# Optimization experiments

Measured on AMD Instinct MI355X. Metric: run time of the kernel, lower is better.

The kernel has to match this reference:

```python
import jax, jax.numpy as jnp
import numpy as np

SAMPLERATE = 22050
N_OCTAVES = 16
N_SAMPLES = 2 ** 15  # 32768
N_EVENTS = 64
BATCH = 4
MIN_HZ = 20
MAX_HZ = 3000
BASE_RESONANCE = 0.01

MIN_FREQ = MIN_HZ / (SAMPLERATE // 2)
MAX_FREQ = MAX_HZ / (SAMPLERATE // 2)
FREQ_RANGE = MAX_FREQ - MIN_FREQ


def setup_inputs() -> dict:
    key = jax.random.key(0)
    k1, k2, k3, k4 = jax.random.split(key, 4)
    return {
        "f0": jax.random.uniform(k1, (BATCH, N_EVENTS, 1), dtype=jnp.float32),
        "decay_coefficients": jax.random.normal(k2, (BATCH, N_EVENTS, 1), dtype=jnp.float32),
        "phase_offsets": jax.random.normal(k3, (BATCH, N_EVENTS, 1), dtype=jnp.float32),
        "freq_spacing": jax.random.uniform(k4, (BATCH, N_EVENTS, 1), dtype=jnp.float32),
    }


def reference(f0, decay_coefficients, phase_offsets, freq_spacing):
    b, e, _ = f0.shape
    f0 = jnp.abs(f0)  # (B, E, 1)

    # computed in the original forward but never used in the output
    _ = jax.nn.sigmoid(phase_offsets) * np.pi

    # exponential_decay(torch.sigmoid(decay_coefficients), ...) -> double sigmoid
    dv = jax.nn.sigmoid(jax.nn.sigmoid(decay_coefficients))  # (B, E, 1)
    resonance_factor = (1.0 - BASE_RESONANCE) * 0.95
    decay = BASE_RESONANCE + dv * resonance_factor
    log_decay = jnp.log(decay + 1e-12)
    # cumsum of the constant over n_frames = n_octaves; F.interpolate to the
    # same size (n_samples=n_octaves in the call) is an identity.
    exp_decays = jnp.exp(jnp.cumsum(
        jnp.broadcast_to(log_decay, (b, e, N_OCTAVES)), axis=-1))  # (B, E, O)

    f0 = (MIN_FREQ + f0 * FREQ_RANGE) * np.pi  # (B, E, 1)
    factors = jnp.cumsum(
        jnp.broadcast_to(freq_spacing, (b, e, N_OCTAVES)), axis=-1)  # (B, E, O)
    f0s = f0 * factors  # (B, E, O) per-octave angular increments

    # cumulative phase over samples, then sin oscillator bank
    phase = jnp.cumsum(
        jnp.broadcast_to(f0s[..., None], (b, e, N_OCTAVES, N_SAMPLES)), axis=-1)
    osc = jnp.sin(phase) * exp_decays[..., None]  # (B, E, O, S)
    osc = jnp.sum(osc, axis=2)  # (B, E, S)

    # max_norm along the sample dim
    mx = jnp.max(jnp.abs(osc), axis=-1, keepdims=True)
    return osc / (mx + 1e-8)
```

## Files before the change

### kernel.cpp

```cpp
#include <hip/hip_runtime.h>
#include <math.h>

#pragma clang fp contract(off)

constexpr int NSAMP = 32768;
constexpr int NROWS = 256;
constexpr int NOCT  = 16;
constexpr int TPB   = 1024;

__device__ __forceinline__ float keepf(float x) {
  asm volatile("" : "+v"(x));
  return x;
}

__global__ __launch_bounds__(TPB, 4) void f0res_kernel(
    const float* __restrict__ f0_in,
    const float* __restrict__ dec_in,
    const float* __restrict__ fs_in,
    float* __restrict__ out)
{
  const int row = blockIdx.x;
  const int t   = threadIdx.x;

  __shared__ float s_tab[NOCT][64];
  __shared__ float s_w[NOCT];
  __shared__ float s_osc[NSAMP];
  __shared__ float s_red[TPB / 64];

  const float f0a = fabsf(f0_in[row]);
  const float dcc = dec_in[row];
  const float fsv = fs_in[row];

  const float MIN_F = (float)(20.0 / 11025.0);
  const float RNG_F = (float)(3000.0 / 11025.0 - 20.0 / 11025.0);
  const float c1    = keepf(f0a * RNG_F);
  const float c2    = keepf(MIN_F + c1);
  const float f0ang = keepf(c2 * (float)M_PI);

  const float sg    = 1.0f / (1.0f + expf(-dcc));
  const float dvv   = 1.0f / (1.0f + expf(-sg));
  const float dvr   = keepf(dvv * 0.9405f);
  const float decay = keepf(0.01f + dvr);
  const float ldv   = logf(decay + 1e-12f);

  if (t < NOCT) {
    const int k = t;
    float fac = 0.0f;
    for (int j = 0; j <= k; ++j) fac = fac + fsv;
    const float x = keepf(f0ang * fac);
    float* tab = s_tab[k];
    float a = 0.0f;
#pragma unroll
    for (int i = 0; i < 16; ++i) { a = a + x;  tab[i]      = a; }
    const float T0 = a; a = 0.0f;
#pragma unroll
    for (int i = 0; i < 16; ++i) { a = a + T0; tab[16 + i] = a; }
    const float T1 = a; a = 0.0f;
#pragma unroll
    for (int i = 0; i < 16; ++i) { a = a + T1; tab[32 + i] = a; }
    const float T2 = a; a = 0.0f;
#pragma unroll
    for (int i = 0; i < 8;  ++i) { a = a + T2; tab[48 + i] = a; }
    float lc = 0.0f;
    for (int j = 0; j <= k; ++j) lc = lc + ldv;
    s_w[k] = expf(lc);
  }
  __syncthreads();

  const float C1 = 6.28125f;
  const float C2 = (float)(6.283185307179586476925287 - 6.28125);
  const float INV2PI = (float)0.159154943091895335768883;

  float lmax = 0.0f;

#pragma unroll
  for (int h = 0; h < 2; ++h) {
    const int m = 2 * t - 1 + h;
    float acc[16];
#pragma unroll
    for (int i = 0; i < 16; ++i) acc[i] = 0.0f;

    for (int k = 0; k < NOCT; ++k) {
      const float* tab = s_tab[k];
      float carry = 0.0f;
      if (m >= 0) {
        carry = tab[16 + (m & 15)];
        const int m2 = (m >> 4) - 1;
        if (m2 >= 0) {
          float p2 = tab[32 + (m2 & 15)];
          const int m3 = (m2 >> 4) - 1;
          if (m3 >= 0) p2 = p2 + tab[48 + m3];
          carry = carry + p2;
        }
      }
      const float w = s_w[k];
      float tv[16];
      *(float4*)&tv[0]  = ((const float4*)tab)[0];
      *(float4*)&tv[4]  = ((const float4*)tab)[1];
      *(float4*)&tv[8]  = ((const float4*)tab)[2];
      *(float4*)&tv[12] = ((const float4*)tab)[3];
#pragma unroll
      for (int i = 0; i < 16; ++i) {
        const float p = tv[i] + carry;
        const float kq = rintf(p * INV2PI);
        float r = __builtin_fmaf(-kq, C1, p);
        r = __builtin_fmaf(-kq, C2, r);
        const float fr = r * INV2PI;
        float sv;
        asm("v_sin_f32 %0, %1" : "=v"(sv) : "v"(fr));
        const float pr = w * sv;
        acc[i] = acc[i] + pr;
      }
    }
#pragma unroll
    for (int i = 0; i < 16; ++i) lmax = fmaxf(lmax, fabsf(acc[i]));
    float4* dst = (float4*)&s_osc[32 * t + 16 * h];
#pragma unroll
    for (int q = 0; q < 4; ++q) {
      float4 v;
      v.x = acc[4*q]; v.y = acc[4*q+1]; v.z = acc[4*q+2]; v.w = acc[4*q+3];
      dst[q] = v;
    }
  }

#pragma unroll
  for (int off = 32; off >= 1; off >>= 1)
    lmax = fmaxf(lmax, __shfl_xor(lmax, off, 64));
  if ((t & 63) == 0) s_red[t >> 6] = lmax;
  __syncthreads();
  float mx = s_red[0];
#pragma unroll
  for (int i = 1; i < TPB / 64; ++i) mx = fmaxf(mx, s_red[i]);
  const float inv = 1.0f / (mx + 1e-8f);

  float4* orow = (float4*)(out + (size_t)row * NSAMP);
  const float4* src = (const float4*)s_osc;
#pragma unroll
  for (int g = 0; g < 8; ++g) {
    float4 v = src[t + 1024 * g];
    v.x *= inv; v.y *= inv; v.z *= inv; v.w *= inv;
    orow[t + 1024 * g] = v;
  }
}

extern "C" void kernel_launch(void* const* d_in, const int* in_sizes, int n_in,
                              void* d_out, int out_size, void* d_ws, size_t ws_size,
                              hipStream_t stream) {
    const float* f0  = (const float*)d_in[0];
    const float* dcc = (const float*)d_in[1];
    const float* fsp = (const float*)d_in[3];
    float* out = (float*)d_out;

    f0res_kernel<<<NROWS, TPB, 0, stream>>>(f0, dcc, fsp, out);
}
```

Baseline: 48.78 us.

## Keep all 32 per-thread outputs in registers and drop the shared staging buffer

Swaps the loop order so the octave loop is outermost: each thread reads a table row's sixteen shared-memory entries once and updates 32 register accumulators. This replaces two 16-sample passes that each re-read the table. The 128 KB shared s_osc buffer goes away, and normalized results are written straight from registers to global memory. Weighted accumulation becomes a fused multiply-add. The costs are higher register pressure under the 1024-thread launch bound, with possible spills, and less coalesced global stores, since each thread now writes its own contiguous 128-byte run.

```diff
diff --git a/kernel.cpp b/kernel.cpp
--- a/kernel.cpp
+++ b/kernel.cpp
@@ -24,7 +24,6 @@
 
   __shared__ float s_tab[NOCT][64];
   __shared__ float s_w[NOCT];
-  __shared__ float s_osc[NSAMP];
   __shared__ float s_red[TPB / 64];
 
   const float f0a = fabsf(f0_in[row]);
@@ -33,9 +32,9 @@
 
   const float MIN_F = (float)(20.0 / 11025.0);
   const float RNG_F = (float)(3000.0 / 11025.0 - 20.0 / 11025.0);
-  const float c1    = keepf(f0a * RNG_F);
-  const float c2    = keepf(MIN_F + c1);
-  const float f0ang = keepf(c2 * (float)M_PI);
+  const float c1s   = keepf(f0a * RNG_F);
+  const float c2s   = keepf(MIN_F + c1s);
+  const float f0ang = keepf(c2s * (float)M_PI);
 
   const float sg    = 1.0f / (1.0f + expf(-dcc));
   const float dvv   = 1.0f / (1.0f + expf(-sg));
@@ -71,58 +70,56 @@
   const float C2 = (float)(6.283185307179586476925287 - 6.28125);
   const float INV2PI = (float)0.159154943091895335768883;
 
-  float lmax = 0.0f;
+  float osc[32];
+#pragma unroll
+  for (int e = 0; e < 32; ++e) osc[e] = 0.0f;
 
+  const int m0 = 2 * t - 1;
+
+#pragma unroll 2
+  for (int k = 0; k < NOCT; ++k) {
+    const float* tab = s_tab[k];
+    float tv[16];
+    *(float4*)&tv[0]  = ((const float4*)tab)[0];
+    *(float4*)&tv[4]  = ((const float4*)tab)[1];
+    *(float4*)&tv[8]  = ((const float4*)tab)[2];
+    *(float4*)&tv[12] = ((const float4*)tab)[3];
+    const float w = s_w[k];
+
+    float carry[2];
 #pragma unroll
-  for (int h = 0; h < 2; ++h) {
-    const int m = 2 * t - 1 + h;
-    float acc[16];
-#pragma unroll
-    for (int i = 0; i < 16; ++i) acc[i] = 0.0f;
-
-    for (int k = 0; k < NOCT; ++k) {
-      const float* tab = s_tab[k];
-      float carry = 0.0f;
+    for (int h = 0; h < 2; ++h) {
+      const int m = m0 + h;
+      float c = 0.0f;
       if (m >= 0) {
-        carry = tab[16 + (m & 15)];
+        c = tab[16 + (m & 15)];
         const int m2 = (m >> 4) - 1;
         if (m2 >= 0) {
           float p2 = tab[32 + (m2 & 15)];
           const int m3 = (m2 >> 4) - 1;
           if (m3 >= 0) p2 = p2 + tab[48 + m3];
-          carry = carry + p2;
+          c = c + p2;
         }
       }
-      const float w = s_w[k];
-      float tv[16];
-      *(float4*)&tv[0]  = ((const float4*)tab)[0];
-      *(float4*)&tv[4]  = ((const float4*)tab)[1];
-      *(float4*)&tv[8]  = ((const float4*)tab)[2];
-      *(float4*)&tv[12] = ((const float4*)tab)[3];
+      carry[h] = c;
+    }
+
 #pragma unroll
-      for (int i = 0; i < 16; ++i) {
-        const float p = tv[i] + carry;
-        const float kq = rintf(p * INV2PI);
-        float r = __builtin_fmaf(-kq, C1, p);
-        r = __builtin_fmaf(-kq, C2, r);
-        const float fr = r * INV2PI;
-        float sv;
-        asm("v_sin_f32 %0, %1" : "=v"(sv) : "v"(fr));
-        const float pr = w * sv;
-        acc[i] = acc[i] + pr;
-      }
-    }
-#pragma unroll
-    for (int i = 0; i < 16; ++i) lmax = fmaxf(lmax, fabsf(acc[i]));
-    float4* dst = (float4*)&s_osc[32 * t + 16 * h];
-#pragma unroll
-    for (int q = 0; q < 4; ++q) {
-      float4 v;
-      v.x = acc[4*q]; v.y = acc[4*q+1]; v.z = acc[4*q+2]; v.w = acc[4*q+3];
-      dst[q] = v;
+    for (int e = 0; e < 32; ++e) {
+      const float p = tv[e & 15] + carry[e >> 4];
+      const float kq = rintf(p * INV2PI);
+      float r = __builtin_fmaf(-kq, C1, p);
+      r = __builtin_fmaf(-kq, C2, r);
+      const float fr = r * INV2PI;
+      float sv;
+      asm("v_sin_f32 %0, %1" : "=v"(sv) : "v"(fr));
+      osc[e] = __builtin_fmaf(w, sv, osc[e]);
     }
   }
 
+  float lmax = 0.0f;
+#pragma unroll
+  for (int e = 0; e < 32; ++e) lmax = fmaxf(lmax, fabsf(osc[e]));
 #pragma unroll
   for (int off = 32; off >= 1; off >>= 1)
     lmax = fmaxf(lmax, __shfl_xor(lmax, off, 64));
@@ -133,13 +130,15 @@
   for (int i = 1; i < TPB / 64; ++i) mx = fmaxf(mx, s_red[i]);
   const float inv = 1.0f / (mx + 1e-8f);
 
-  float4* orow = (float4*)(out + (size_t)row * NSAMP);
-  const float4* src = (const float4*)s_osc;
+  float4* o4 = (float4*)(out + (size_t)row * NSAMP + 32 * t);
 #pragma unroll
-  for (int g = 0; g < 8; ++g) {
-    float4 v = src[t + 1024 * g];
-    v.x *= inv; v.y *= inv; v.z *= inv; v.w *= inv;
-    orow[t + 1024 * g] = v;
+  for (int q = 0; q < 8; ++q) {
+    float4 v;
+    v.x = osc[4 * q + 0] * inv;
+    v.y = osc[4 * q + 1] * inv;
+    v.z = osc[4 * q + 2] * inv;
+    v.w = osc[4 * q + 3] * inv;
+    o4[q] = v;
   }
 }
 
```

Result: slower. 50.80 us (+4.1%).

## Split into segment-parallel oscillator kernel plus atomic-max normalization pass

Applied to the files above, without the earlier changes.

Each row is now computed by eight 256-thread blocks, each covering 4096 samples, instead of one 1024-thread block. This drops the 128 KB shared-memory staging buffer so more blocks can be resident per CU. Un-normalized samples are written straight to global memory in a permuted layout, and a per-row max is combined through a global atomicMax on the float bit pattern. A second kernel then reads the samples back, un-permutes them and scales them. The cost is an extra memset, a second launch and a global read-write round trip over the whole output.

```diff
diff --git a/kernel.cpp b/kernel.cpp
--- a/kernel.cpp
+++ b/kernel.cpp
@@ -6,25 +6,29 @@
 constexpr int NSAMP = 32768;
 constexpr int NROWS = 256;
 constexpr int NOCT  = 16;
-constexpr int TPB   = 1024;
+constexpr int SEGS  = 8;
+constexpr int TPB   = 256;
+constexpr int GRID1 = NROWS * SEGS;
 
 __device__ __forceinline__ float keepf(float x) {
   asm volatile("" : "+v"(x));
   return x;
 }
 
-__global__ __launch_bounds__(TPB, 4) void f0res_kernel(
+__global__ __launch_bounds__(TPB, 8) void f0res_k1(
     const float* __restrict__ f0_in,
     const float* __restrict__ dec_in,
     const float* __restrict__ fs_in,
-    float* __restrict__ out)
+    float* __restrict__ out,
+    unsigned int* __restrict__ rowmax)
 {
-  const int row = blockIdx.x;
+  const int bid = blockIdx.x;
+  const int row = bid >> 3;
+  const int seg = bid & 7;
   const int t   = threadIdx.x;
 
   __shared__ float s_tab[NOCT][64];
   __shared__ float s_w[NOCT];
-  __shared__ float s_osc[NSAMP];
   __shared__ float s_red[TPB / 64];
 
   const float f0a = fabsf(f0_in[row]);
@@ -33,9 +37,9 @@
 
   const float MIN_F = (float)(20.0 / 11025.0);
   const float RNG_F = (float)(3000.0 / 11025.0 - 20.0 / 11025.0);
-  const float c1    = keepf(f0a * RNG_F);
-  const float c2    = keepf(MIN_F + c1);
-  const float f0ang = keepf(c2 * (float)M_PI);
+  const float c1s   = keepf(f0a * RNG_F);
+  const float c2s   = keepf(MIN_F + c1s);
+  const float f0ang = keepf(c2s * (float)M_PI);
 
   const float sg    = 1.0f / (1.0f + expf(-dcc));
   const float dvv   = 1.0f / (1.0f + expf(-sg));
@@ -71,75 +75,98 @@
   const float C2 = (float)(6.283185307179586476925287 - 6.28125);
   const float INV2PI = (float)0.159154943091895335768883;
 
-  float lmax = 0.0f;
+  const int m = seg * 256 + t - 1;
+
+  float osc[16];
+#pragma unroll
+  for (int e = 0; e < 16; ++e) osc[e] = 0.0f;
+
+  for (int k = 0; k < NOCT; ++k) {
+    const float* tab = s_tab[k];
+    float tv[16];
+    *(float4*)&tv[0]  = ((const float4*)tab)[0];
+    *(float4*)&tv[4]  = ((const float4*)tab)[1];
+    *(float4*)&tv[8]  = ((const float4*)tab)[2];
+    *(float4*)&tv[12] = ((const float4*)tab)[3];
+    const float w = s_w[k];
+
+    float carry = 0.0f;
+    if (m >= 0) {
+      carry = tab[16 + (m & 15)];
+      const int m2 = (m >> 4) - 1;
+      if (m2 >= 0) {
+        float p2 = tab[32 + (m2 & 15)];
+        const int m3 = (m2 >> 4) - 1;
+        if (m3 >= 0) p2 = p2 + tab[48 + m3];
+        carry = carry + p2;
+      }
+    }
 
 #pragma unroll
-  for (int h = 0; h < 2; ++h) {
-    const int m = 2 * t - 1 + h;
-    float acc[16];
-#pragma unroll
-    for (int i = 0; i < 16; ++i) acc[i] = 0.0f;
-
-    for (int k = 0; k < NOCT; ++k) {
-      const float* tab = s_tab[k];
-      float carry = 0.0f;
-      if (m >= 0) {
-        carry = tab[16 + (m & 15)];
-        const int m2 = (m >> 4) - 1;
-        if (m2 >= 0) {
-          float p2 = tab[32 + (m2 & 15)];
-          const int m3 = (m2 >> 4) - 1;
-          if (m3 >= 0) p2 = p2 + tab[48 + m3];
-          carry = carry + p2;
-        }
-      }
-      const float w = s_w[k];
-      float tv[16];
-      *(float4*)&tv[0]  = ((const float4*)tab)[0];
-      *(float4*)&tv[4]  = ((const float4*)tab)[1];
-      *(float4*)&tv[8]  = ((const float4*)tab)[2];
-      *(float4*)&tv[12] = ((const float4*)tab)[3];
-#pragma unroll
-      for (int i = 0; i < 16; ++i) {
-        const float p = tv[i] + carry;
-        const float kq = rintf(p * INV2PI);
-        float r = __builtin_fmaf(-kq, C1, p);
-        r = __builtin_fmaf(-kq, C2, r);
-        const float fr = r * INV2PI;
-        float sv;
-        asm("v_sin_f32 %0, %1" : "=v"(sv) : "v"(fr));
-        const float pr = w * sv;
-        acc[i] = acc[i] + pr;
-      }
-    }
-#pragma unroll
-    for (int i = 0; i < 16; ++i) lmax = fmaxf(lmax, fabsf(acc[i]));
-    float4* dst = (float4*)&s_osc[32 * t + 16 * h];
-#pragma unroll
-    for (int q = 0; q < 4; ++q) {
-      float4 v;
-      v.x = acc[4*q]; v.y = acc[4*q+1]; v.z = acc[4*q+2]; v.w = acc[4*q+3];
-      dst[q] = v;
+    for (int e = 0; e < 16; ++e) {
+      const float p = tv[e] + carry;
+      const float kq = rintf(p * INV2PI);
+      float r = __builtin_fmaf(-kq, C1, p);
+      r = __builtin_fmaf(-kq, C2, r);
+      const float fr = r * INV2PI;
+      float sv;
+      asm("v_sin_f32 %0, %1" : "=v"(sv) : "v"(fr));
+      osc[e] = __builtin_fmaf(w, sv, osc[e]);
     }
   }
 
+  float lmax = 0.0f;
+#pragma unroll
+  for (int e = 0; e < 16; ++e) lmax = fmaxf(lmax, fabsf(osc[e]));
 #pragma unroll
   for (int off = 32; off >= 1; off >>= 1)
     lmax = fmaxf(lmax, __shfl_xor(lmax, off, 64));
   if ((t & 63) == 0) s_red[t >> 6] = lmax;
   __syncthreads();
-  float mx = s_red[0];
+  if (t == 0) {
+    float mx = s_red[0];
 #pragma unroll
-  for (int i = 1; i < TPB / 64; ++i) mx = fmaxf(mx, s_red[i]);
+    for (int i = 1; i < TPB / 64; ++i) mx = fmaxf(mx, s_red[i]);
+    atomicMax(&rowmax[row], __float_as_uint(mx));
+  }
+
+  float4* o4 = (float4*)out + (size_t)bid * 1024;
+#pragma unroll
+  for (int q = 0; q < 4; ++q) {
+    float4 v;
+    v.x = osc[4 * q + 0];
+    v.y = osc[4 * q + 1];
+    v.z = osc[4 * q + 2];
+    v.w = osc[4 * q + 3];
+    o4[q * 256 + t] = v;
+  }
+}
+
+__global__ __launch_bounds__(TPB, 8) void f0res_k2(
+    float* __restrict__ out,
+    const unsigned int* __restrict__ rowmax)
+{
+  const int bid = blockIdx.x;
+  const int t   = threadIdx.x;
+  const int row = bid >> 3;
+
+  const float mx  = __uint_as_float(rowmax[row]);
   const float inv = 1.0f / (mx + 1e-8f);
 
-  float4* orow = (float4*)(out + (size_t)row * NSAMP);
-  const float4* src = (const float4*)s_osc;
+  float4* base = (float4*)out + (size_t)bid * 1024;
+
+  float4 v[4];
 #pragma unroll
-  for (int g = 0; g < 8; ++g) {
-    float4 v = src[t + 1024 * g];
-    v.x *= inv; v.y *= inv; v.z *= inv; v.w *= inv;
-    orow[t + 1024 * g] = v;
+  for (int q = 0; q < 4; ++q) {
+    const int s = (t & 3) * 256 + 64 * q + (t >> 2);
+    v[q] = base[s];
+  }
+  __syncthreads();
+#pragma unroll
+  for (int q = 0; q < 4; ++q) {
+    float4 x = v[q];
+    x.x *= inv; x.y *= inv; x.z *= inv; x.w *= inv;
+    base[q * 256 + t] = x;
   }
 }
 
@@ -150,6 +177,9 @@
     const float* dcc = (const float*)d_in[1];
     const float* fsp = (const float*)d_in[3];
     float* out = (float*)d_out;
+    unsigned int* rowmax = (unsigned int*)d_ws;
 
-    f0res_kernel<<<NROWS, TPB, 0, stream>>>(f0, dcc, fsp, out);
+    hipMemsetAsync(rowmax, 0, NROWS * sizeof(unsigned int), stream);
+    f0res_k1<<<GRID1, TPB, 0, stream>>>(f0, dcc, fsp, out, rowmax);
+    f0res_k2<<<GRID1, TPB, 0, stream>>>(out, rowmax);
 }
```

Result: slower. 56.69 us (+16.2%).
